# Performance work log

Measured on AMD Instinct MI355X. Metric: run time of the kernel, lower is better.

Reference implementation:

```python
import jax, jax.numpy as jnp
import numpy as np

EPS = 1e-5
L0_BETA = 2.0 / 3.0   # unused in deterministic path
L0_GAMMA = -0.1
L0_ZETA = 1.1
NEG_SLOPE = 0.2


def _bn(v, axes, g, b, pshape):
    # batch-norm using batch statistics (training-mode math, biased var like torch)
    mean = jnp.mean(v, axis=axes, keepdims=True)
    var = jnp.var(v, axis=axes, keepdims=True)
    return (v - mean) * jax.lax.rsqrt(var + EPS) * g.reshape(pshape) + b.reshape(pshape)


def setup_inputs() -> dict:
    key = jax.random.key(0)
    ks = jax.random.split(key, 4)
    n, c, t, h, w = 32, 1024, 32, 7, 7
    n_nodes = 128
    return {
        "x": jax.random.normal(ks[0], (n, c, t, h, w), jnp.float32),
        "nodes": jax.random.normal(ks[1], (n_nodes, c), jnp.float32),
        "g1": jnp.ones((c,), jnp.float32), "b1": jnp.zeros((c,), jnp.float32),
        "g2": jnp.ones((c,), jnp.float32), "b2": jnp.zeros((c,), jnp.float32),
        "g3": jnp.ones((n_nodes,), jnp.float32), "b3": jnp.zeros((n_nodes,), jnp.float32),
        "W": jax.random.normal(ks[2], (c, c), jnp.float32) * (1.0 / np.sqrt(c)),
        "bW": jnp.zeros((c,), jnp.float32),
        "loc": jnp.ones((1,), jnp.float32),  # hard-concrete location param (penalty_loc_mean=1)
        "g6": jnp.ones((c,), jnp.float32), "b6": jnp.zeros((c,), jnp.float32),
    }


def reference(x, nodes, g1, b1, g2, b2, g3, b3, W, bW, loc, g6, b6):
    # x: (n,c,t,h,w), nodes: (K,c)
    # bn_1: BatchNorm3d over channel c
    x = _bn(x, (0, 2, 3, 4), g1, b1, (1, -1, 1, 1, 1))
    # bn_2: BatchNorm1d on (K,c) -> per-channel stats across nodes
    nd = _bn(nodes, (0,), g2, b2, (1, -1))
    # linear_1
    nd = nd @ W.T + bW
    # bn_3: pl.BatchNorm(n_nodes, dim=0) -> per-node stats across channels
    nd = _bn(nd, (1,), g3, b3, (-1, 1))
    # tensor_product_1: f (n,h,w,K,t)
    f = jnp.einsum('ncthw,kc->nhwkt', x, nd)
    # L0Norm hard-concrete gate (deterministic/eval path)
    s_bar = jax.nn.sigmoid(loc) * (L0_ZETA - L0_GAMMA) + L0_GAMMA
    gate = jnp.clip(s_bar, 0.0, 1.0)
    alpha = f * gate
    # tensor_product_2: y (n,c,t,h,w)
    y = jnp.einsum('nhwkt,kc->ncthw', alpha, nd)
    # bn_6 + LeakyReLU(0.2)
    y = _bn(y, (0, 2, 3, 4), g6, b6, (1, -1, 1, 1, 1))
    return jnp.where(y >= 0, y, NEG_SLOPE * y)
```

## Files before the change

kernel.cpp:

```cpp
#include <hip/hip_runtime.h>
#include <hip/hip_bf16.h>

#define NB 32
#define CC 1024
#define SS 1568
#define KK 128
#define NCOL 448
#define EPSV 1e-5f
#define XP_P 132
#define NSB3 224

typedef __attribute__((ext_vector_type(8))) short bf16x8;
typedef __attribute__((ext_vector_type(4))) short bf16x4v;
typedef __attribute__((ext_vector_type(4))) float f32x4;

__device__ __forceinline__ unsigned short f2bf(float f) {
  union { float f; unsigned u; } v; v.f = f;
  return (unsigned short)((v.u + 0x7fffu + ((v.u >> 16) & 1u)) >> 16);
}
__device__ __forceinline__ float bf2f(unsigned short h) {
  union { unsigned u; float f; } v; v.u = ((unsigned)h) << 16; return v.f;
}

__global__ __launch_bounds__(512) void xpose_stats(
    const float* __restrict__ x, unsigned short* __restrict__ xT,
    float* __restrict__ p1s, float* __restrict__ p1q) {
  __shared__ float lt[64 * XP_P];
  int sb = blockIdx.x, cc = blockIdx.y, n = blockIdx.z;
  int t = threadIdx.x;
  int s0 = sb * 112, c0 = cc * 64;
  const float* xp = x + ((size_t)n * CC + c0) * SS + s0;
  #pragma unroll
  for (int j = 0; j < 4; j++) {
    int idx = t + 512 * j;
    if (idx < 1792) {
      int r = idx / 28, q = idx % 28;
      float4 v = *(const float4*)(xp + (size_t)r * SS + 4 * q);
      *(float4*)&lt[r * XP_P + 4 * (q ^ (r >> 3))] = v;
    }
  }
  __syncthreads();
  if (t < 256) {
    int r = t >> 2, m = t & 3;
    float s = 0.f, sq = 0.f;
    #pragma unroll
    for (int i = 0; i < 7; i++) {
      int b = m * 7 + i;
      float4 v = *(const float4*)&lt[r * XP_P + 4 * (b ^ (r >> 3))];
      s  += v.x + v.y + v.z + v.w;
      sq += v.x * v.x + v.y * v.y + v.z * v.z + v.w * v.w;
    }
    s += __shfl_xor(s, 1); sq += __shfl_xor(sq, 1);
    s += __shfl_xor(s, 2); sq += __shfl_xor(sq, 2);
    if (m == 0) {
      int col = n * 14 + sb;
      p1s[(size_t)(c0 + r) * NCOL + col] = s;
      p1q[(size_t)(c0 + r) * NCOL + col] = sq;
    }
  }
  if (t < 448) {
    int co = t & 7, sl = t >> 3;
    #pragma unroll
    for (int j = 0; j < 2; j++) {
      int sloc = sl + 56 * j;
      int s = s0 + sloc;
      bf16x8 pk;
      #pragma unroll
      for (int i = 0; i < 8; i++) {
        int r = co * 8 + i;
        pk[i] = (short)f2bf(lt[r * XP_P + 4 * ((sloc >> 2) ^ co) + (sloc & 3)]);
      }
      size_t off = (size_t)n * 1605632 +
                   (size_t)((s >> 4) * 32 + (cc * 2 + (co >> 2))) * 512 +
                   (s & 15) * 32 + (co & 3) * 8;
      *(bf16x8*)(xT + off) = pk;
    }
  }
}

__global__ void bn1_fin(const float* __restrict__ p1s, const float* __restrict__ p1q,
                        const float* __restrict__ g1, const float* __restrict__ b1,
                        float* a1, float* c1) {
  __shared__ float red[4][32][2];
  int t = threadIdx.x;
  int cl = t & 31, part = t >> 5, w = t >> 6;
  int c = blockIdx.x * 32 + cl;
  const float4* ps = (const float4*)(p1s + (size_t)c * NCOL + part * 56);
  const float4* pq = (const float4*)(p1q + (size_t)c * NCOL + part * 56);
  float s = 0.f, sq = 0.f;
  #pragma unroll
  for (int i = 0; i < 14; i++) {
    float4 v = ps[i]; s += v.x + v.y + v.z + v.w;
    float4 u = pq[i]; sq += u.x + u.y + u.z + u.w;
  }
  s += __shfl_xor(s, 32); sq += __shfl_xor(sq, 32);
  if ((t & 63) < 32) { red[w][cl][0] = s; red[w][cl][1] = sq; }
  __syncthreads();
  if (t < 32) {
    float st = red[0][t][0] + red[1][t][0] + red[2][t][0] + red[3][t][0];
    float qt = red[0][t][1] + red[1][t][1] + red[2][t][1] + red[3][t][1];
    float inv = 1.f / ((float)NB * SS);
    float m = st * inv, var = qt * inv - m * m;
    float r = rsqrtf(var + EPSV);
    float a = g1[c] * r;
    a1[c] = a; c1[c] = b1[c] - m * a;
  }
}

__global__ void bn2_nh(const float* __restrict__ nodes, const float* __restrict__ g2,
                       const float* __restrict__ b2, unsigned short* __restrict__ nh) {
  __shared__ float sred[4][8][2];
  __shared__ float bc[8][2];
  int t = threadIdx.x;
  int cl = t & 7, kq = t >> 3, w = t >> 6;
  int c = blockIdx.x * 8 + cl;
  float s = 0.f, sq = 0.f;
  #pragma unroll
  for (int i = 0; i < 4; i++) {
    float v = nodes[(size_t)(kq + 32 * i) * CC + c];
    s += v; sq += v * v;
  }
  s += __shfl_xor(s, 8);  sq += __shfl_xor(sq, 8);
  s += __shfl_xor(s, 16); sq += __shfl_xor(sq, 16);
  s += __shfl_xor(s, 32); sq += __shfl_xor(sq, 32);
  if ((t & 63) < 8) { sred[w][cl][0] = s; sred[w][cl][1] = sq; }
  __syncthreads();
  if (t < 8) {
    float st = sred[0][t][0] + sred[1][t][0] + sred[2][t][0] + sred[3][t][0];
    float qt = sred[0][t][1] + sred[1][t][1] + sred[2][t][1] + sred[3][t][1];
    float inv = 1.f / (float)KK;
    float m = st * inv, var = qt * inv - m * m;
    float r = rsqrtf(var + EPSV);
    float a = g2[blockIdx.x * 8 + t] * r;
    bc[t][0] = a; bc[t][1] = b2[blockIdx.x * 8 + t] - m * a;
  }
  __syncthreads();
  float a = bc[cl][0], cc2 = bc[cl][1];
  #pragma unroll
  for (int i = 0; i < 4; i++) {
    int k = kq + 32 * i;
    nh[(size_t)k * CC + c] = f2bf(nodes[(size_t)k * CC + c] * a + cc2);
  }
}

__global__ __launch_bounds__(256) void linear_mfma(
    const unsigned short* __restrict__ nh, const float* __restrict__ Wm,
    const float* __restrict__ bW, float* __restrict__ Lb) {
  int jt = blockIdx.x, mt = blockIdx.y;
  int t = threadIdx.x, w = t >> 6, lane = t & 63, g = lane >> 4, l15 = lane & 15;
  int krow = mt * 64 + w * 16 + l15;
  f32x4 acc[2];
  acc[0] = (f32x4){0.f,0.f,0.f,0.f}; acc[1] = (f32x4){0.f,0.f,0.f,0.f};
  #pragma unroll 4
  for (int c0 = 0; c0 < CC; c0 += 32) {
    bf16x8 af = *(const bf16x8*)(nh + (size_t)krow * CC + c0 + g * 8);
    #pragma unroll
    for (int nf = 0; nf < 2; nf++) {
      const float* wr = Wm + (size_t)(jt * 32 + nf * 16 + l15) * CC + c0 + g * 8;
      float4 v0 = *(const float4*)wr, v1 = *(const float4*)(wr + 4);
      bf16x8 bfr;
      bfr[0] = (short)f2bf(v0.x); bfr[1] = (short)f2bf(v0.y);
      bfr[2] = (short)f2bf(v0.z); bfr[3] = (short)f2bf(v0.w);
      bfr[4] = (short)f2bf(v1.x); bfr[5] = (short)f2bf(v1.y);
      bfr[6] = (short)f2bf(v1.z); bfr[7] = (short)f2bf(v1.w);
      acc[nf] = __builtin_amdgcn_mfma_f32_16x16x32_bf16(af, bfr, acc[nf], 0, 0, 0);
    }
  }
  #pragma unroll
  for (int nf = 0; nf < 2; nf++) {
    int j = jt * 32 + nf * 16 + l15;
    float bwv = bW[j];
    #pragma unroll
    for (int r = 0; r < 4; r++)
      Lb[(size_t)(mt * 64 + w * 16 + g * 4 + r) * CC + j] = acc[nf][r] + bwv;
  }
}

__global__ void bn3_pack(const float* __restrict__ Lb, const float* __restrict__ g3,
                         const float* __restrict__ b3, const float* __restrict__ loc,
                         const float* __restrict__ a1, const float* __restrict__ c1,
                         unsigned short* __restrict__ ndA2, unsigned short* __restrict__ Mt,
                         unsigned short* __restrict__ MtL, float* __restrict__ Cst) {
  __shared__ float red[8];
  int k = blockIdx.x, t = threadIdx.x, w = t >> 6;
  float vv[4];
  float s = 0.f, sq = 0.f;
  for (int i = 0; i < 4; i++) {
    float v = Lb[(size_t)k * CC + t + 256 * i];
    vv[i] = v; s += v; sq += v * v;
  }
  for (int m = 1; m < 64; m <<= 1) { s += __shfl_xor(s, m); sq += __shfl_xor(sq, m); }
  if ((t & 63) == 0) { red[w] = s; red[4 + w] = sq; }
  __syncthreads();
  s  = red[0] + red[1] + red[2] + red[3];
  sq = red[4] + red[5] + red[6] + red[7];
  float inv = 1.f / (float)CC;
  float m3 = s * inv, var = sq * inv - m3 * m3;
  float r = rsqrtf(var + EPSV);
  float a = g3[k] * r, cc3 = b3[k] - m3 * a;
  float lv = loc[0];
  float gate = 1.f / (1.f + __expf(-lv)) * 1.2f - 0.1f;
  gate = fminf(fmaxf(gate, 0.f), 1.f);
  float cs = 0.f;
  for (int i = 0; i < 4; i++) {
    int j = t + 256 * i;
    float nd = vv[i] * a + cc3;
    unsigned short ndb = f2bf(nd * a1[j]);
    unsigned short mtb = f2bf(gate * nd);
    ndA2[(size_t)((k >> 4) * 32 + (j >> 5)) * 512 + (k & 15) * 32 + ((j >> 3) & 3) * 8 + (j & 7)] = ndb;
    Mt[(size_t)((j >> 4) * 4 + (k >> 5)) * 512 + (j & 15) * 32 + ((k >> 3) & 3) * 8 + (k & 7)] = mtb;
    MtL[(size_t)j * KK + k] = mtb;
    cs += c1[j] * nd;
  }
  for (int m = 1; m < 64; m <<= 1) cs += __shfl_xor(cs, m);
  __syncthreads();
  if ((t & 63) == 0) red[w] = cs;
  __syncthreads();
  if (t == 0) Cst[k] = red[0] + red[1] + red[2] + red[3];
}

__global__ __launch_bounds__(256) void gemm1(
    const unsigned short* __restrict__ ndA2, const unsigned short* __restrict__ xT,
    const float* __restrict__ Cst, unsigned short* __restrict__ GT) {
  int sb = blockIdx.x;
  int n  = blockIdx.y;
  int t = threadIdx.x, w = t >> 6, lane = t & 63, g = lane >> 4, l15 = lane & 15;
  f32x4 acc[2][2];
  for (int m = 0; m < 2; m++)
    for (int nf = 0; nf < 2; nf++) acc[m][nf] = (f32x4){0.f, 0.f, 0.f, 0.f};
  int lofs = l15 * 32 + g * 8;
  const unsigned short* xb = xT + (size_t)n * 1605632;
  #pragma unroll 4
  for (int cc2 = 0; cc2 < 32; cc2++) {
    bf16x8 af[2], bfr[2];
    #pragma unroll
    for (int m = 0; m < 2; m++)
      af[m] = *(const bf16x8*)(ndA2 + (size_t)((w * 2 + m) * 32 + cc2) * 512 + lofs);
    #pragma unroll
    for (int nf = 0; nf < 2; nf++)
      bfr[nf] = *(const bf16x8*)(xb + (size_t)((sb * 2 + nf) * 32 + cc2) * 512 + lofs);
    #pragma unroll
    for (int m = 0; m < 2; m++)
      #pragma unroll
      for (int nf = 0; nf < 2; nf++)
        acc[m][nf] = __builtin_amdgcn_mfma_f32_16x16x32_bf16(af[m], bfr[nf], acc[m][nf], 0, 0, 0);
  }
  unsigned short* gtn = GT + (size_t)n * 200704;
  #pragma unroll
  for (int nf = 0; nf < 2; nf++) {
    #pragma unroll
    for (int m = 0; m < 2; m++) {
      int kb = w * 32 + m * 16 + g * 4;
      float4 cst = *(const float4*)(Cst + kb);
      bf16x4v ov;
      ov[0] = (short)f2bf(acc[m][nf][0] + cst.x);
      ov[1] = (short)f2bf(acc[m][nf][1] + cst.y);
      ov[2] = (short)f2bf(acc[m][nf][2] + cst.z);
      ov[3] = (short)f2bf(acc[m][nf][3] + cst.w);
      int g2 = m * 2 + (g >> 1);
      int e0 = (g & 1) * 4;
      *(bf16x4v*)(gtn + (size_t)((sb * 2 + nf) * 4 + w) * 512 + l15 * 32 + g2 * 8 + e0) = ov;
    }
  }
}

__global__ __launch_bounds__(256) void gram(const unsigned short* __restrict__ GT,
                                            float* __restrict__ part) {
  __shared__ float lf[112 * 128];
  int b = blockIdx.x, t = threadIdx.x;
  int k1b = t >> 4, k2b = t & 15;
  float acc[8][8];
  float gsum[8];
  #pragma unroll
  for (int i = 0; i < 8; i++) {
    gsum[i] = 0.f;
    #pragma unroll
    for (int j = 0; j < 8; j++) acc[i][j] = 0.f;
  }
  for (int chunk = 0; chunk < 2; chunk++) {
    int St0 = b * 14 + chunk * 7;
    #pragma unroll
    for (int it = 0; it < 7; it++) {
      int u = t + 256 * it;
      int Stl = u >> 8, rem = u & 255;
      bf16x8 v = *(const bf16x8*)(GT + (size_t)(St0 + Stl) * 2048 + rem * 8);
      int sl = Stl * 16 + ((rem & 63) >> 2);
      int kk = (rem >> 6) * 32 + (rem & 3) * 8;
      float4 f0, f1;
      f0.x = bf2f((unsigned short)v[0]); f0.y = bf2f((unsigned short)v[1]);
      f0.z = bf2f((unsigned short)v[2]); f0.w = bf2f((unsigned short)v[3]);
      f1.x = bf2f((unsigned short)v[4]); f1.y = bf2f((unsigned short)v[5]);
      f1.z = bf2f((unsigned short)v[6]); f1.w = bf2f((unsigned short)v[7]);
      *(float4*)&lf[sl * 128 + kk] = f0;
      *(float4*)&lf[sl * 128 + kk + 4] = f1;
    }
    __syncthreads();
    for (int sl = 0; sl < 112; sl++) {
      float4 a0 = *(const float4*)&lf[sl * 128 + k1b * 8];
      float4 a1 = *(const float4*)&lf[sl * 128 + k1b * 8 + 4];
      float4 b0 = *(const float4*)&lf[sl * 128 + k2b * 8];
      float4 b1 = *(const float4*)&lf[sl * 128 + k2b * 8 + 4];
      float a[8]  = {a0.x, a0.y, a0.z, a0.w, a1.x, a1.y, a1.z, a1.w};
      float bb[8] = {b0.x, b0.y, b0.z, b0.w, b1.x, b1.y, b1.z, b1.w};
      #pragma unroll
      for (int i = 0; i < 8; i++)
        #pragma unroll
        for (int j = 0; j < 8; j++) acc[i][j] += a[i] * bb[j];
      if (k1b == 0) {
        #pragma unroll
        for (int j = 0; j < 8; j++) gsum[j] += bb[j];
      }
    }
    __syncthreads();
  }
  float* pb = part + (size_t)b * 16512;
  #pragma unroll
  for (int i = 0; i < 8; i++) {
    int k1 = k1b * 8 + i;
    *(float4*)(pb + k1 * 128 + k2b * 8)     = (float4){acc[i][0], acc[i][1], acc[i][2], acc[i][3]};
    *(float4*)(pb + k1 * 128 + k2b * 8 + 4) = (float4){acc[i][4], acc[i][5], acc[i][6], acc[i][7]};
  }
  if (k1b == 0) {
    *(float4*)(pb + 16384 + k2b * 8)     = (float4){gsum[0], gsum[1], gsum[2], gsum[3]};
    *(float4*)(pb + 16384 + k2b * 8 + 4) = (float4){gsum[4], gsum[5], gsum[6], gsum[7]};
  }
}

__global__ void gram_reduceA(const float* __restrict__ part, float* __restrict__ partB) {
  int e = blockIdx.x * 256 + threadIdx.x;
  if (e >= 16512) return;
  int p0 = blockIdx.y * 56;
  float s = 0.f;
  #pragma unroll 8
  for (int p = p0; p < p0 + 56; p++) s += part[(size_t)p * 16512 + e];
  partB[(size_t)blockIdx.y * 16512 + e] = s;
}
__global__ void gram_reduceB(const float* __restrict__ partB, float* __restrict__ Cov) {
  int e = blockIdx.x * 256 + threadIdx.x;
  if (e >= 16512) return;
  Cov[e] = partB[e] + partB[16512 + e] + partB[2 * 16512 + e] + partB[3 * 16512 + e];
}

__global__ __launch_bounds__(256) void bn6stats(
    const float* __restrict__ Cov, const unsigned short* __restrict__ MtL,
    const float* __restrict__ g6, const float* __restrict__ b6,
    float* a6, float* c6) {
  __shared__ float covL[16384];
  __shared__ float mL[8 * 128];
  __shared__ float gbL[128];
  int b = blockIdx.x, t = threadIdx.x;
  int c0 = b * 8;
  #pragma unroll
  for (int i = 0; i < 16; i++) {
    int u = t + 256 * i;
    *(float4*)&covL[u * 4] = *(const float4*)(Cov + u * 4);
  }
  if (t < 128) {
    int row = t >> 4, unit = t & 15;
    bf16x8 v = *(const bf16x8*)(MtL + (size_t)(c0 + row) * KK + unit * 8);
    #pragma unroll
    for (int j = 0; j < 8; j++) mL[row * 128 + unit * 8 + j] = bf2f((unsigned short)v[j]);
  }
  if (t < 32) *(float4*)&gbL[t * 4] = *(const float4*)(Cov + 16384 + t * 4);
  __syncthreads();
  int cl = t >> 5, kq = t & 31;
  float4 m4 = *(const float4*)&mL[cl * 128 + kq * 4];
  float4 g4 = *(const float4*)&gbL[kq * 4];
  float mv = m4.x * g4.x + m4.y * g4.y + m4.z * g4.z + m4.w * g4.w;
  float vv = 0.f;
  for (int k = 0; k < 128; k++) {
    float4 c4 = *(const float4*)&covL[k * 128 + kq * 4];
    float mk = mL[cl * 128 + k];
    vv += mk * (c4.x * m4.x + c4.y * m4.y + c4.z * m4.z + c4.w * m4.w);
  }
  for (int msk = 1; msk < 32; msk <<= 1) { mv += __shfl_xor(mv, msk); vv += __shfl_xor(vv, msk); }
  if (kq == 0) {
    int c = c0 + cl;
    float inv = 1.f / ((float)NB * SS);
    float mean = mv * inv, var = vv * inv - mean * mean;
    float r = rsqrtf(var + EPSV);
    float a = g6[c] * r;
    a6[c] = a; c6[c] = b6[c] - mean * a;
  }
}

__global__ __launch_bounds__(256) void gemm2(
    const unsigned short* __restrict__ Mt, const unsigned short* __restrict__ GT,
    const float* __restrict__ a6, const float* __restrict__ c6,
    float* __restrict__ out) {
  int id = blockIdx.x;
  int xcd = id & 7;
  int mid = id >> 3;
  int ct  = mid & 7;
  int p   = (mid >> 3) * 8 + xcd;
  int sb  = p % 14, n = p / 14;
  int t = threadIdx.x, w = t >> 6, lane = t & 63, g = lane >> 4, l15 = lane & 15;
  f32x4 acc[2][7];
  for (int m = 0; m < 2; m++)
    for (int nf = 0; nf < 7; nf++) acc[m][nf] = (f32x4){0.f, 0.f, 0.f, 0.f};
  int lofs = l15 * 32 + g * 8;
  const unsigned short* gtb = GT + (size_t)n * 200704;
  #pragma unroll
  for (int ks = 0; ks < 4; ks++) {
    bf16x8 af[2];
    #pragma unroll
    for (int m = 0; m < 2; m++)
      af[m] = *(const bf16x8*)(Mt + (size_t)((ct * 8 + w * 2 + m) * 4 + ks) * 512 + lofs);
    #pragma unroll
    for (int nf = 0; nf < 7; nf++) {
      bf16x8 bfr = *(const bf16x8*)(gtb + (size_t)((sb * 7 + nf) * 4 + ks) * 512 + lofs);
      #pragma unroll
      for (int m = 0; m < 2; m++)
        acc[m][nf] = __builtin_amdgcn_mfma_f32_16x16x32_bf16(af[m], bfr, acc[m][nf], 0, 0, 0);
    }
  }
  #pragma unroll
  for (int m = 0; m < 2; m++) {
    int cb = ct * 128 + w * 32 + m * 16 + g * 4;
    float4 av = *(const float4*)(a6 + cb);
    float4 cv = *(const float4*)(c6 + cb);
    #pragma unroll
    for (int nf = 0; nf < 7; nf++) {
      int s = sb * 112 + nf * 16 + l15;
      #pragma unroll
      for (int r = 0; r < 4; r++) {
        float a = (r == 0) ? av.x : (r == 1) ? av.y : (r == 2) ? av.z : av.w;
        float cc = (r == 0) ? cv.x : (r == 1) ? cv.y : (r == 2) ? cv.z : cv.w;
        float v = acc[m][nf][r] * a + cc;
        v = v >= 0.f ? v : 0.2f * v;
        __builtin_nontemporal_store(v, &out[((size_t)(n * CC + cb + r)) * SS + s]);
      }
    }
  }
}

extern "C" void kernel_launch(void* const* d_in, const int* in_sizes, int n_in,
                              void* d_out, int out_size, void* d_ws, size_t ws_size,
                              hipStream_t stream) {
  const float* x     = (const float*)d_in[0];
  const float* nodes = (const float*)d_in[1];
  const float* g1 = (const float*)d_in[2];
  const float* b1 = (const float*)d_in[3];
  const float* g2 = (const float*)d_in[4];
  const float* b2 = (const float*)d_in[5];
  const float* g3 = (const float*)d_in[6];
  const float* b3 = (const float*)d_in[7];
  const float* Wm = (const float*)d_in[8];
  const float* bW = (const float*)d_in[9];
  const float* loc = (const float*)d_in[10];
  const float* g6 = (const float*)d_in[11];
  const float* b6 = (const float*)d_in[12];
  float* out = (float*)d_out;
  char* ws = (char*)d_ws;

  float* p1s = (float*)(ws + 0);
  float* p1q = (float*)(ws + 1835008);
  float* a1  = (float*)(ws + 3670016);
  float* c1  = (float*)(ws + 3674112);
  float* Cst = (float*)(ws + 3678208);
  unsigned short* nh   = (unsigned short*)(ws + 3682304);
  float* Lb  = (float*)(ws + 3944448);
  unsigned short* ndA2 = (unsigned short*)(ws + 4468736);
  unsigned short* Mt   = (unsigned short*)(ws + 4730880);
  unsigned short* MtL  = (unsigned short*)(ws + 4993024);
  float* a6  = (float*)(ws + 5255168);
  float* c6  = (float*)(ws + 5259264);
  float* Cov = (float*)(ws + 5263360);
  float* gramP = (float*)(ws + 5329920);
  unsigned short* GT = (unsigned short*)(ws + 20124672);
  unsigned short* xT = (unsigned short*)(ws + 32969728);
  float* partB = (float*)(ws + 135730176);

  xpose_stats<<<dim3(14, 16, NB), dim3(512), 0, stream>>>(x, xT, p1s, p1q);
  bn2_nh<<<dim3(128), dim3(256), 0, stream>>>(nodes, g2, b2, nh);
  linear_mfma<<<dim3(32, 2), dim3(256), 0, stream>>>(nh, Wm, bW, Lb);
  bn1_fin<<<dim3(32), dim3(256), 0, stream>>>(p1s, p1q, g1, b1, a1, c1);
  bn3_pack<<<dim3(KK), dim3(256), 0, stream>>>(Lb, g3, b3, loc, a1, c1, ndA2, Mt, MtL, Cst);
  gemm1<<<dim3(49, NB), dim3(256), 0, stream>>>(ndA2, xT, Cst, GT);
  gram<<<dim3(NSB3), dim3(256), 0, stream>>>(GT, gramP);
  gram_reduceA<<<dim3(65, 4), dim3(256), 0, stream>>>(gramP, partB);
  gram_reduceB<<<dim3(65), dim3(256), 0, stream>>>(partB, Cov);
  bn6stats<<<dim3(128), dim3(256), 0, stream>>>(Cov, MtL, g6, b6, a6, c6);
  gemm2<<<dim3(3584), dim3(256), 0, stream>>>(Mt, GT, a6, c6, out);
}
```

Measured before the change: 278.1 us.

## Fuse small stats kernels, compute BN1 stats during load, add nontemporal hints

The BN1 partial sums are now accumulated while x is loaded from global memory, using a small shared-memory reduction, instead of in a second pass over the LDS tile. bn2_nh and bn1_fin are merged into one launch, and gram_reduceB is folded into bn6stats, which sums the four partB slices itself. Nontemporal loads and stores are added on the x read, the xT write and the xT read in gemm1. This cuts two kernel launches and some LDS traffic. In exchange every bn6stats block now repeats the 4-way partial sum, and the nontemporal hints may hurt cache reuse of xT.

Measured after the change: 306.6 us. +10.3%, slower.

```diff
diff --git a/kernel.cpp b/kernel.cpp
--- a/kernel.cpp
+++ b/kernel.cpp
@@ -26,37 +26,33 @@
     const float* __restrict__ x, unsigned short* __restrict__ xT,
     float* __restrict__ p1s, float* __restrict__ p1q) {
   __shared__ float lt[64 * XP_P];
+  __shared__ float axs[64][8], axq[64][8];
   int sb = blockIdx.x, cc = blockIdx.y, n = blockIdx.z;
   int t = threadIdx.x;
   int s0 = sb * 112, c0 = cc * 64;
   const float* xp = x + ((size_t)n * CC + c0) * SS + s0;
-  #pragma unroll
-  for (int j = 0; j < 4; j++) {
-    int idx = t + 512 * j;
-    if (idx < 1792) {
-      int r = idx / 28, q = idx % 28;
-      float4 v = *(const float4*)(xp + (size_t)r * SS + 4 * q);
-      *(float4*)&lt[r * XP_P + 4 * (q ^ (r >> 3))] = v;
-    }
+  if (t < 448) {
+    int r = t / 7, j7 = t % 7;
+    int qb = j7 * 4;
+    float s = 0.f, sq = 0.f;
+    #pragma unroll
+    for (int j = 0; j < 4; j++) {
+      int q = qb + j;
+      f32x4 v = __builtin_nontemporal_load((const f32x4*)(xp + (size_t)r * SS + 4 * q));
+      *(f32x4*)&lt[r * XP_P + 4 * (q ^ (r >> 3))] = v;
+      s  += v[0] + v[1] + v[2] + v[3];
+      sq += v[0] * v[0] + v[1] * v[1] + v[2] * v[2] + v[3] * v[3];
+    }
+    axs[r][j7] = s; axq[r][j7] = sq;
   }
   __syncthreads();
-  if (t < 256) {
-    int r = t >> 2, m = t & 3;
+  if (t < 64) {
     float s = 0.f, sq = 0.f;
     #pragma unroll
-    for (int i = 0; i < 7; i++) {
-      int b = m * 7 + i;
-      float4 v = *(const float4*)&lt[r * XP_P + 4 * (b ^ (r >> 3))];
-      s  += v.x + v.y + v.z + v.w;
-      sq += v.x * v.x + v.y * v.y + v.z * v.z + v.w * v.w;
-    }
-    s += __shfl_xor(s, 1); sq += __shfl_xor(sq, 1);
-    s += __shfl_xor(s, 2); sq += __shfl_xor(sq, 2);
-    if (m == 0) {
-      int col = n * 14 + sb;
-      p1s[(size_t)(c0 + r) * NCOL + col] = s;
-      p1q[(size_t)(c0 + r) * NCOL + col] = sq;
-    }
+    for (int j = 0; j < 7; j++) { s += axs[t][j]; sq += axq[t][j]; }
+    int col = n * 14 + sb;
+    p1s[(size_t)(c0 + t) * NCOL + col] = s;
+    p1q[(size_t)(c0 + t) * NCOL + col] = sq;
   }
   if (t < 448) {
     int co = t & 7, sl = t >> 3;
@@ -73,73 +69,75 @@
       size_t off = (size_t)n * 1605632 +
                    (size_t)((s >> 4) * 32 + (cc * 2 + (co >> 2))) * 512 +
                    (s & 15) * 32 + (co & 3) * 8;
-      *(bf16x8*)(xT + off) = pk;
-    }
-  }
-}
-
-__global__ void bn1_fin(const float* __restrict__ p1s, const float* __restrict__ p1q,
-                        const float* __restrict__ g1, const float* __restrict__ b1,
-                        float* a1, float* c1) {
-  __shared__ float red[4][32][2];
-  int t = threadIdx.x;
-  int cl = t & 31, part = t >> 5, w = t >> 6;
-  int c = blockIdx.x * 32 + cl;
-  const float4* ps = (const float4*)(p1s + (size_t)c * NCOL + part * 56);
-  const float4* pq = (const float4*)(p1q + (size_t)c * NCOL + part * 56);
-  float s = 0.f, sq = 0.f;
-  #pragma unroll
-  for (int i = 0; i < 14; i++) {
-    float4 v = ps[i]; s += v.x + v.y + v.z + v.w;
-    float4 u = pq[i]; sq += u.x + u.y + u.z + u.w;
-  }
-  s += __shfl_xor(s, 32); sq += __shfl_xor(sq, 32);
-  if ((t & 63) < 32) { red[w][cl][0] = s; red[w][cl][1] = sq; }
-  __syncthreads();
-  if (t < 32) {
-    float st = red[0][t][0] + red[1][t][0] + red[2][t][0] + red[3][t][0];
-    float qt = red[0][t][1] + red[1][t][1] + red[2][t][1] + red[3][t][1];
-    float inv = 1.f / ((float)NB * SS);
-    float m = st * inv, var = qt * inv - m * m;
-    float r = rsqrtf(var + EPSV);
-    float a = g1[c] * r;
-    a1[c] = a; c1[c] = b1[c] - m * a;
-  }
-}
-
-__global__ void bn2_nh(const float* __restrict__ nodes, const float* __restrict__ g2,
-                       const float* __restrict__ b2, unsigned short* __restrict__ nh) {
+      __builtin_nontemporal_store(pk, (bf16x8*)(xT + off));
+    }
+  }
+}
+
+__global__ void prep_stats(const float* __restrict__ nodes, const float* __restrict__ g2,
+                           const float* __restrict__ b2, unsigned short* __restrict__ nh,
+                           const float* __restrict__ p1s, const float* __restrict__ p1q,
+                           const float* __restrict__ g1, const float* __restrict__ b1,
+                           float* a1, float* c1) {
   __shared__ float sred[4][8][2];
   __shared__ float bc[8][2];
-  int t = threadIdx.x;
-  int cl = t & 7, kq = t >> 3, w = t >> 6;
-  int c = blockIdx.x * 8 + cl;
-  float s = 0.f, sq = 0.f;
-  #pragma unroll
-  for (int i = 0; i < 4; i++) {
-    float v = nodes[(size_t)(kq + 32 * i) * CC + c];
-    s += v; sq += v * v;
-  }
-  s += __shfl_xor(s, 8);  sq += __shfl_xor(sq, 8);
-  s += __shfl_xor(s, 16); sq += __shfl_xor(sq, 16);
-  s += __shfl_xor(s, 32); sq += __shfl_xor(sq, 32);
-  if ((t & 63) < 8) { sred[w][cl][0] = s; sred[w][cl][1] = sq; }
-  __syncthreads();
-  if (t < 8) {
-    float st = sred[0][t][0] + sred[1][t][0] + sred[2][t][0] + sred[3][t][0];
-    float qt = sred[0][t][1] + sred[1][t][1] + sred[2][t][1] + sred[3][t][1];
-    float inv = 1.f / (float)KK;
-    float m = st * inv, var = qt * inv - m * m;
-    float r = rsqrtf(var + EPSV);
-    float a = g2[blockIdx.x * 8 + t] * r;
-    bc[t][0] = a; bc[t][1] = b2[blockIdx.x * 8 + t] - m * a;
-  }
-  __syncthreads();
-  float a = bc[cl][0], cc2 = bc[cl][1];
-  #pragma unroll
-  for (int i = 0; i < 4; i++) {
-    int k = kq + 32 * i;
-    nh[(size_t)k * CC + c] = f2bf(nodes[(size_t)k * CC + c] * a + cc2);
+  __shared__ float red1[4][32][2];
+  int t = threadIdx.x, w = t >> 6;
+  if (blockIdx.x < 128) {
+    int blk = blockIdx.x;
+    int cl = t & 7, kq = t >> 3;
+    int c = blk * 8 + cl;
+    float s = 0.f, sq = 0.f;
+    #pragma unroll
+    for (int i = 0; i < 4; i++) {
+      float v = nodes[(size_t)(kq + 32 * i) * CC + c];
+      s += v; sq += v * v;
+    }
+    s += __shfl_xor(s, 8);  sq += __shfl_xor(sq, 8);
+    s += __shfl_xor(s, 16); sq += __shfl_xor(sq, 16);
+    s += __shfl_xor(s, 32); sq += __shfl_xor(sq, 32);
+    if ((t & 63) < 8) { sred[w][cl][0] = s; sred[w][cl][1] = sq; }
+    __syncthreads();
+    if (t < 8) {
+      float st = sred[0][t][0] + sred[1][t][0] + sred[2][t][0] + sred[3][t][0];
+      float qt = sred[0][t][1] + sred[1][t][1] + sred[2][t][1] + sred[3][t][1];
+      float inv = 1.f / (float)KK;
+      float m = st * inv, var = qt * inv - m * m;
+      float r = rsqrtf(var + EPSV);
+      float a = g2[blk * 8 + t] * r;
+      bc[t][0] = a; bc[t][1] = b2[blk * 8 + t] - m * a;
+    }
+    __syncthreads();
+    float a = bc[cl][0], cc2 = bc[cl][1];
+    #pragma unroll
+    for (int i = 0; i < 4; i++) {
+      int k = kq + 32 * i;
+      nh[(size_t)k * CC + c] = f2bf(nodes[(size_t)k * CC + c] * a + cc2);
+    }
+  } else {
+    int blk = blockIdx.x - 128;
+    int cl = t & 31, part = t >> 5;
+    int c = blk * 32 + cl;
+    const float4* ps = (const float4*)(p1s + (size_t)c * NCOL + part * 56);
+    const float4* pq = (const float4*)(p1q + (size_t)c * NCOL + part * 56);
+    float s = 0.f, sq = 0.f;
+    #pragma unroll
+    for (int i = 0; i < 14; i++) {
+      float4 v = ps[i]; s += v.x + v.y + v.z + v.w;
+      float4 u = pq[i]; sq += u.x + u.y + u.z + u.w;
+    }
+    s += __shfl_xor(s, 32); sq += __shfl_xor(sq, 32);
+    if ((t & 63) < 32) { red1[w][cl][0] = s; red1[w][cl][1] = sq; }
+    __syncthreads();
+    if (t < 32) {
+      float st = red1[0][t][0] + red1[1][t][0] + red1[2][t][0] + red1[3][t][0];
+      float qt = red1[0][t][1] + red1[1][t][1] + red1[2][t][1] + red1[3][t][1];
+      float inv = 1.f / ((float)NB * SS);
+      float m = st * inv, var = qt * inv - m * m;
+      float r = rsqrtf(var + EPSV);
+      float a = g1[c] * r;
+      a1[c] = a; c1[c] = b1[c] - m * a;
+    }
   }
 }
 
@@ -238,7 +236,7 @@
       af[m] = *(const bf16x8*)(ndA2 + (size_t)((w * 2 + m) * 32 + cc2) * 512 + lofs);
     #pragma unroll
     for (int nf = 0; nf < 2; nf++)
-      bfr[nf] = *(const bf16x8*)(xb + (size_t)((sb * 2 + nf) * 32 + cc2) * 512 + lofs);
+      bfr[nf] = __builtin_nontemporal_load((const bf16x8*)(xb + (size_t)((sb * 2 + nf) * 32 + cc2) * 512 + lofs));
     #pragma unroll
     for (int m = 0; m < 2; m++)
       #pragma unroll
@@ -335,14 +333,9 @@
   for (int p = p0; p < p0 + 56; p++) s += part[(size_t)p * 16512 + e];
   partB[(size_t)blockIdx.y * 16512 + e] = s;
 }
-__global__ void gram_reduceB(const float* __restrict__ partB, float* __restrict__ Cov) {
-  int e = blockIdx.x * 256 + threadIdx.x;
-  if (e >= 16512) return;
-  Cov[e] = partB[e] + partB[16512 + e] + partB[2 * 16512 + e] + partB[3 * 16512 + e];
-}
 
 __global__ __launch_bounds__(256) void bn6stats(
-    const float* __restrict__ Cov, const unsigned short* __restrict__ MtL,
+    const float* __restrict__ partB, const unsigned short* __restrict__ MtL,
     const float* __restrict__ g6, const float* __restrict__ b6,
     float* a6, float* c6) {
   __shared__ float covL[16384];
@@ -352,8 +345,13 @@
   int c0 = b * 8;
   #pragma unroll
   for (int i = 0; i < 16; i++) {
-    int u = t + 256 * i;
-    *(float4*)&covL[u * 4] = *(const float4*)(Cov + u * 4);
+    int u = (t + 256 * i) * 4;
+    float4 va = *(const float4*)(partB + u);
+    float4 vb = *(const float4*)(partB + 16512 + u);
+    float4 vc = *(const float4*)(partB + 2 * 16512 + u);
+    float4 vd = *(const float4*)(partB + 3 * 16512 + u);
+    *(float4*)&covL[u] = (float4){va.x + vb.x + vc.x + vd.x, va.y + vb.y + vc.y + vd.y,
+                                  va.z + vb.z + vc.z + vd.z, va.w + vb.w + vc.w + vd.w};
   }
   if (t < 128) {
     int row = t >> 4, unit = t & 15;
@@ -361,7 +359,15 @@
     #pragma unroll
     for (int j = 0; j < 8; j++) mL[row * 128 + unit * 8 + j] = bf2f((unsigned short)v[j]);
   }
-  if (t < 32) *(float4*)&gbL[t * 4] = *(const float4*)(Cov + 16384 + t * 4);
+  if (t < 32) {
+    int u = 16384 + t * 4;
+    float4 va = *(const float4*)(partB + u);
+    float4 vb = *(const float4*)(partB + 16512 + u);
+    float4 vc = *(const float4*)(partB + 2 * 16512 + u);
+    float4 vd = *(const float4*)(partB + 3 * 16512 + u);
+    *(float4*)&gbL[t * 4] = (float4){va.x + vb.x + vc.x + vd.x, va.y + vb.y + vc.y + vd.y,
+                                     va.z + vb.z + vc.z + vd.z, va.w + vb.w + vc.w + vd.w};
+  }
   __syncthreads();
   int cl = t >> 5, kq = t & 31;
   float4 m4 = *(const float4*)&mL[cl * 128 + kq * 4];
@@ -465,21 +471,18 @@
   unsigned short* MtL  = (unsigned short*)(ws + 4993024);
   float* a6  = (float*)(ws + 5255168);
   float* c6  = (float*)(ws + 5259264);
-  float* Cov = (float*)(ws + 5263360);
   float* gramP = (float*)(ws + 5329920);
   unsigned short* GT = (unsigned short*)(ws + 20124672);
   unsigned short* xT = (unsigned short*)(ws + 32969728);
   float* partB = (float*)(ws + 135730176);
 
   xpose_stats<<<dim3(14, 16, NB), dim3(512), 0, stream>>>(x, xT, p1s, p1q);
-  bn2_nh<<<dim3(128), dim3(256), 0, stream>>>(nodes, g2, b2, nh);
+  prep_stats<<<dim3(160), dim3(256), 0, stream>>>(nodes, g2, b2, nh, p1s, p1q, g1, b1, a1, c1);
   linear_mfma<<<dim3(32, 2), dim3(256), 0, stream>>>(nh, Wm, bW, Lb);
-  bn1_fin<<<dim3(32), dim3(256), 0, stream>>>(p1s, p1q, g1, b1, a1, c1);
   bn3_pack<<<dim3(KK), dim3(256), 0, stream>>>(Lb, g3, b3, loc, a1, c1, ndA2, Mt, MtL, Cst);
   gemm1<<<dim3(49, NB), dim3(256), 0, stream>>>(ndA2, xT, Cst, GT);
   gram<<<dim3(NSB3), dim3(256), 0, stream>>>(GT, gramP);
   gram_reduceA<<<dim3(65, 4), dim3(256), 0, stream>>>(gramP, partB);
-  gram_reduceB<<<dim3(65), dim3(256), 0, stream>>>(partB, Cov);
-  bn6stats<<<dim3(128), dim3(256), 0, stream>>>(Cov, MtL, g6, b6, a6, c6);
+  bn6stats<<<dim3(128), dim3(256), 0, stream>>>(partB, MtL, g6, b6, a6, c6);
   gemm2<<<dim3(3584), dim3(256), 0, stream>>>(Mt, GT, a6, c6, out);
 }
```
